# Kernel optimization log

Hardware: AMD Instinct MI355X
Metric: run time of the kernel (lower is better)

The kernel has to match this reference:

```python
import jax, jax.numpy as jnp
import numpy as np

N_NODES = 100000


def _gcn_layer(h, W, b, src, dst, norm, n):
    # h: [N, Fin] -> [N, Fout]; normalized scatter-add aggregation (GCNConv)
    hw = h @ W
    msg = norm[:, None] * hw[src]
    out = jax.ops.segment_sum(msg, dst, num_segments=n)
    return out + b


def setup_inputs() -> dict:
    key = jax.random.key(0)
    k = jax.random.split(key, 10)
    N, E, P, F = N_NODES, 3200000, 500000, 128
    x = jax.random.normal(k[0], (N, F), dtype=jnp.float32)
    edge_index = jax.random.randint(k[1], (2, E), 0, N, dtype=jnp.int64)
    pred_edges = jax.random.randint(k[2], (P, 2), 0, N, dtype=jnp.int64)
    # Glorot-ish init for learned params
    W1 = jax.random.normal(k[3], (F, 16), dtype=jnp.float32) / np.sqrt(F)
    b1 = jnp.zeros((16,), dtype=jnp.float32)
    W2 = jax.random.normal(k[4], (16, 8), dtype=jnp.float32) / np.sqrt(16.0)
    b2 = jnp.zeros((8,), dtype=jnp.float32)
    Wl = jax.random.normal(k[5], (8, 1), dtype=jnp.float32) / np.sqrt(8.0)
    bl = jnp.zeros((1,), dtype=jnp.float32)
    return {"x": x, "edge_index": edge_index, "pred_edges": pred_edges,
            "W1": W1, "b1": b1, "W2": W2, "b2": b2, "Wl": Wl, "bl": bl}


def reference(x, edge_index, pred_edges, W1, b1, W2, b2, Wl, bl):
    n = x.shape[0]
    # GCN norm with self-loops: A_hat = D^{-1/2}(A+I)D^{-1/2}
    loop = jnp.arange(n, dtype=edge_index.dtype)
    src = jnp.concatenate([edge_index[0], loop])
    dst = jnp.concatenate([edge_index[1], loop])
    deg = jax.ops.segment_sum(jnp.ones_like(dst, dtype=x.dtype), dst, num_segments=n)
    dinv = jnp.where(deg > 0, jax.lax.rsqrt(deg), 0.0)
    norm = dinv[src] * dinv[dst]

    h = _gcn_layer(x, W1, b1, src, dst, norm, n)   # [N, 16]
    h = _gcn_layer(h, W2, b2, src, dst, norm, n)   # [N, 8]
    z = jax.nn.sigmoid(h @ Wl + bl)                # [N, 1]
    m = z[pred_edges]                              # [P, 2, 1]
    pred = m[:, 0, 0] * m[:, 1, 0]                 # [P]
    return pred
```

## Files before the change

kernel.cpp:

```cpp
#include <hip/hip_runtime.h>
#include <hip/hip_fp16.h>
#include <math.h>

#define BSHIFT 8
#define BUCK   256
#define TILE   8192
#define CAP    12288

typedef _Float16 f16x2 __attribute__((ext_vector_type(2)));
typedef _Float16 f16x4 __attribute__((ext_vector_type(4)));
typedef _Float16 f16x8 __attribute__((ext_vector_type(8)));
typedef float    f32x4 __attribute__((ext_vector_type(4)));


__global__ __launch_bounds__(256) void k_curinit(int* __restrict__ bcursor, int nbuk) {
    int b = blockIdx.x * 256 + threadIdx.x;
    if (b < nbuk) bcursor[b] = b * CAP;
}

__global__ __launch_bounds__(1024) void k_binscatter(const int* __restrict__ src,
                                                     const int* __restrict__ dst,
                                                     int* __restrict__ bcursor,
                                                     int* __restrict__ binned, int E, int nbuk) {
    __shared__ int            payload[TILE];
    __shared__ unsigned short bid16[TILE];
    __shared__ int cnt[512];
    __shared__ int lstart[512];
    __shared__ int gbase[512];
    __shared__ int wsum[8];
    int t = threadIdx.x;
    int tile0 = blockIdx.x * TILE;
    int tileE = min(TILE, E - tile0);
    if (t < 512) cnt[t] = 0;
    __syncthreads();
    int d[8], s[8];
    int base = t * 8;
    if (base + 8 <= tileE) {
        const int4* d4 = (const int4*)(dst + tile0 + base);
        const int4* s4 = (const int4*)(src + tile0 + base);
        int4 da = d4[0], db = d4[1];
        int4 sa = s4[0], sb = s4[1];
        d[0] = da.x; d[1] = da.y; d[2] = da.z; d[3] = da.w;
        d[4] = db.x; d[5] = db.y; d[6] = db.z; d[7] = db.w;
        s[0] = sa.x; s[1] = sa.y; s[2] = sa.z; s[3] = sa.w;
        s[4] = sb.x; s[5] = sb.y; s[6] = sb.z; s[7] = sb.w;
    } else {
#pragma unroll
        for (int q = 0; q < 8; ++q) {
            int idx = base + q;
            if (idx < tileE) { d[q] = dst[tile0 + idx]; s[q] = src[tile0 + idx]; }
            else d[q] = -1;
        }
    }
#pragma unroll
    for (int q = 0; q < 8; ++q)
        if (d[q] >= 0) atomicAdd(&cnt[d[q] >> BSHIFT], 1);
    __syncthreads();
    int c = 0, ex = 0;
    if (t < 512) {
        c = cnt[t];
        int v = c;
#pragma unroll
        for (int off = 1; off < 64; off <<= 1) {
            int u = __shfl_up(v, off, 64);
            if ((t & 63) >= off) v += u;
        }
        if ((t & 63) == 63) wsum[t >> 6] = v;
        ex = v - c;
    }
    __syncthreads();
    if (t == 0) {
        int run = 0;
#pragma unroll
        for (int w = 0; w < 8; ++w) { int u = wsum[w]; wsum[w] = run; run += u; }
    }
    __syncthreads();
    if (t < 512) {
        ex += wsum[t >> 6];
        gbase[t] = c ? atomicAdd(&bcursor[t], c) : 0;
        lstart[t] = ex;
        cnt[t] = ex;
    }
    __syncthreads();
#pragma unroll
    for (int q = 0; q < 8; ++q) {
        if (d[q] >= 0) {
            int b = d[q] >> BSHIFT;
            int lp = atomicAdd(&cnt[b], 1);
            payload[lp] = ((d[q] & (BUCK - 1)) << 17) | s[q];
            bid16[lp] = (unsigned short)b;
        }
    }
    __syncthreads();
    for (int k = t; k < tileE; k += 1024) {
        int b = bid16[k];
        int ga = gbase[b] + (k - lstart[b]);
        if (ga < (b + 1) * CAP)
            binned[ga] = payload[k];
    }
}

__global__ __launch_bounds__(1024) void k_sortbucket(const int* __restrict__ bcursor,
                                                     const int* __restrict__ binned,
                                                     int* __restrict__ csr_src,
                                                     int* __restrict__ rowstart,
                                                     int* __restrict__ rowend,
                                                     float* __restrict__ dinv, int N) {
    __shared__ int cnt[BUCK];
    __shared__ int cur[BUCK];
    __shared__ int wsum[4];
    int b = blockIdx.x, t = threadIdx.x;
    if (t < BUCK) cnt[t] = 0;
    __syncthreads();
    int beg = b * CAP;
    int end = min(bcursor[b], beg + CAP);
    int v[12];
#pragma unroll
    for (int q = 0; q < 12; ++q) {
        int e = beg + q * 1024 + t;
        v[q] = (e < end) ? binned[e] : -1;
    }
#pragma unroll
    for (int q = 0; q < 12; ++q)
        if (v[q] >= 0) atomicAdd(&cnt[v[q] >> 17], 1);
    __syncthreads();
    int c = 0, ex = 0;
    if (t < BUCK) {
        c = cnt[t];
        int s = c;
#pragma unroll
        for (int off = 1; off < 64; off <<= 1) {
            int u = __shfl_up(s, off, 64);
            if ((t & 63) >= off) s += u;
        }
        if ((t & 63) == 63) wsum[t >> 6] = s;
        ex = s - c;
    }
    __syncthreads();
    if (t == 0) {
        int run = 0;
#pragma unroll
        for (int w = 0; w < 4; ++w) { int u = wsum[w]; wsum[w] = run; run += u; }
    }
    __syncthreads();
    if (t < BUCK) {
        ex += wsum[t >> 6];
        cur[t] = ex;
        int node = b * BUCK + t;
        if (node < N) {
            rowstart[node] = beg + ex;
            rowend[node]   = beg + ex + c;
            dinv[node] = rsqrtf((float)(c + 1));
        }
    }
    __syncthreads();
#pragma unroll
    for (int q = 0; q < 12; ++q) {
        if (v[q] >= 0) {
            int pos = atomicAdd(&cur[v[q] >> 17], 1);
            csr_src[beg + pos] = v[q] & 0x1FFFF;
        }
    }
}


__global__ __launch_bounds__(256) void k_gemm1(const float* __restrict__ x,
                                               const float* __restrict__ W1,
                                               const float* __restrict__ dinv,
                                               __half* __restrict__ hw1h, int N) {
    __shared__ _Float16 sX[64 * 136];
    __shared__ _Float16 sW[16 * 136];
    __shared__ float    sDi[64];
    __shared__ _Float16 sOut[64 * 16];
    int t = threadIdx.x;
    int row0 = blockIdx.x * 64;
    for (int e = t; e < 2048; e += 256) {
        int n = e & 15, k = e >> 4;
        sW[n * 136 + k] = (_Float16)W1[k * 16 + n];
    }
    const float4* x4 = (const float4*)x;
#pragma unroll
    for (int q = 0; q < 8; ++q) {
        int e = q * 256 + t;
        int r = e >> 5, c4 = e & 31;
        int gr = row0 + r;
        float4 v = (gr < N) ? x4[(size_t)gr * 32 + c4] : make_float4(0.f, 0.f, 0.f, 0.f);
        f16x4 hv = {(_Float16)v.x, (_Float16)v.y, (_Float16)v.z, (_Float16)v.w};
        *(f16x4*)&sX[r * 136 + c4 * 4] = hv;
    }
    if (t < 64) sDi[t] = (row0 + t < N) ? dinv[row0 + t] : 0.f;
    __syncthreads();
    int w = t >> 6, l = t & 63;
    int m = l & 15, quad = l >> 4;
    f32x4 acc = {0.f, 0.f, 0.f, 0.f};
#pragma unroll
    for (int kc = 0; kc < 4; ++kc) {
        f16x8 a = *(const f16x8*)&sX[(w * 16 + m) * 136 + kc * 32 + quad * 8];
        f16x8 b = *(const f16x8*)&sW[m * 136 + kc * 32 + quad * 8];
        acc = __builtin_amdgcn_mfma_f32_16x16x32_f16(a, b, acc, 0, 0, 0);
    }
#pragma unroll
    for (int r = 0; r < 4; ++r) {
        int nl = w * 16 + quad * 4 + r;
        sOut[nl * 16 + m] = (_Float16)(acc[r] * sDi[nl]);
    }
    __syncthreads();
    int nn = t >> 2, ch = t & 3;
    int gn = row0 + nn;
    if (gn < N)
        *(float2*)&hw1h[(size_t)gn * 16 + ch * 4] = *(float2*)&sOut[nn * 16 + ch * 4];
}

__global__ __launch_bounds__(256) void k_agg1c(const int* __restrict__ rowstart,
                                               const int* __restrict__ rowend,
                                               const int* __restrict__ csr_src,
                                               const f16x8* __restrict__ hw1v,
                                               const float* __restrict__ W2,
                                               const float* __restrict__ b1,
                                               __half* __restrict__ hw2h, int N) {
    __shared__ float sW[128], sb[16];
    int t = threadIdx.x;
    if (t < 128) sW[t] = W2[t];
    if (t < 16)  sb[t] = b1[t];
    __syncthreads();
    int q = t >> 2, j = t & 3;
    int i = blockIdx.x * 64 + q;
    if (i >= N) return;
    int beg = rowstart[i], end = rowend[i];
    int deg = end - beg;
    float di = rsqrtf((float)(deg + 1));
    float a[16];
#pragma unroll
    for (int d = 0; d < 16; ++d) a[d] = 0.f;
    int nfull = deg >> 4;
    int base0 = beg + 4 * j;
    int s4[4];
    if (nfull > 0) {
#pragma unroll
        for (int m = 0; m < 4; ++m) s4[m] = csr_src[base0 + m];
    }
    for (int ch = 0; ch < nfull; ++ch) {
        f16x8 lo[4], hi[4];
#pragma unroll
        for (int m = 0; m < 4; ++m) {
            lo[m] = hw1v[2 * (size_t)s4[m]];
            hi[m] = hw1v[2 * (size_t)s4[m] + 1];
        }
        int sn[4];
        if (ch + 1 < nfull) {
#pragma unroll
            for (int m = 0; m < 4; ++m) sn[m] = csr_src[base0 + (ch + 1) * 16 + m];
        }
#pragma unroll
        for (int m = 0; m < 4; ++m) {
#pragma unroll
            for (int d = 0; d < 8; ++d) {
                a[d]     += (float)lo[m][d];
                a[8 + d] += (float)hi[m][d];
            }
        }
        if (ch + 1 < nfull) {
#pragma unroll
            for (int m = 0; m < 4; ++m) s4[m] = sn[m];
        }
    }
    if (deg & 15) {
        int cb = beg + nfull * 16 + 4 * j;
        int   sr[4];
        float wr[4];
#pragma unroll
        for (int m = 0; m < 4; ++m) {
            int c = cb + m;
            bool ok = c < end;
            sr[m] = ok ? csr_src[c] : i;
            wr[m] = ok ? 1.f : 0.f;
        }
        f16x8 lo[4], hi[4];
#pragma unroll
        for (int m = 0; m < 4; ++m) {
            lo[m] = hw1v[2 * (size_t)sr[m]];
            hi[m] = hw1v[2 * (size_t)sr[m] + 1];
        }
#pragma unroll
        for (int m = 0; m < 4; ++m) {
#pragma unroll
            for (int d = 0; d < 8; ++d) {
                a[d]     += wr[m] * (float)lo[m][d];
                a[8 + d] += wr[m] * (float)hi[m][d];
            }
        }
    }
    if (j == 0) {
        f16x8 lo = hw1v[2 * (size_t)i];
        f16x8 hi = hw1v[2 * (size_t)i + 1];
#pragma unroll
        for (int d = 0; d < 8; ++d) {
            a[d]     += (float)lo[d];
            a[8 + d] += (float)hi[d];
        }
    }
#pragma unroll
    for (int d = 0; d < 16; ++d) a[d] += __shfl_xor(a[d], 1, 4);
#pragma unroll
    for (int d = 0; d < 16; ++d) a[d] += __shfl_xor(a[d], 2, 4);
    float o0 = 0.f, o1 = 0.f;
#pragma unroll
    for (int k = 0; k < 16; ++k) {
        float hv = di * a[k] + sb[k];
        o0 += hv * sW[k * 8 + 2 * j];
        o1 += hv * sW[k * 8 + 2 * j + 1];
    }
    f16x2 ho = {(_Float16)(di * o0), (_Float16)(di * o1)};
    *(f16x2*)&hw2h[(size_t)i * 8 + 2 * j] = ho;
}

__global__ __launch_bounds__(256) void k_agg2c(const int* __restrict__ rowstart,
                                               const int* __restrict__ rowend,
                                               const int* __restrict__ csr_src,
                                               const f16x8* __restrict__ hw2v,
                                               const float* __restrict__ Wl,
                                               const float* __restrict__ b2,
                                               const float* __restrict__ bl,
                                               float* __restrict__ z, int N) {
    __shared__ float sW[8], sb[8], sbl;
    int t = threadIdx.x;
    if (t < 8) { sW[t] = Wl[t]; sb[t] = b2[t]; }
    if (t == 0) sbl = bl[0];
    __syncthreads();
    int q = t >> 2, j = t & 3;
    int i = blockIdx.x * 64 + q;
    if (i >= N) return;
    int beg = rowstart[i], end = rowend[i];
    int deg = end - beg;
    float di = rsqrtf((float)(deg + 1));
    float a[8];
#pragma unroll
    for (int d = 0; d < 8; ++d) a[d] = 0.f;
    int nfull = deg >> 4;
    int base0 = beg + 4 * j;
    int s4[4];
    if (nfull > 0) {
#pragma unroll
        for (int m = 0; m < 4; ++m) s4[m] = csr_src[base0 + m];
    }
    for (int ch = 0; ch < nfull; ++ch) {
        f16x8 gv[4];
#pragma unroll
        for (int m = 0; m < 4; ++m) gv[m] = hw2v[(size_t)s4[m]];
        int sn[4];
        if (ch + 1 < nfull) {
#pragma unroll
            for (int m = 0; m < 4; ++m) sn[m] = csr_src[base0 + (ch + 1) * 16 + m];
        }
#pragma unroll
        for (int m = 0; m < 4; ++m)
#pragma unroll
            for (int d = 0; d < 8; ++d) a[d] += (float)gv[m][d];
        if (ch + 1 < nfull) {
#pragma unroll
            for (int m = 0; m < 4; ++m) s4[m] = sn[m];
        }
    }
    if (deg & 15) {
        int cb = beg + nfull * 16 + 4 * j;
        int   sr[4];
        float wr[4];
#pragma unroll
        for (int m = 0; m < 4; ++m) {
            int c = cb + m;
            bool ok = c < end;
            sr[m] = ok ? csr_src[c] : i;
            wr[m] = ok ? 1.f : 0.f;
        }
        f16x8 gv[4];
#pragma unroll
        for (int m = 0; m < 4; ++m) gv[m] = hw2v[(size_t)sr[m]];
#pragma unroll
        for (int m = 0; m < 4; ++m)
#pragma unroll
            for (int d = 0; d < 8; ++d) a[d] += wr[m] * (float)gv[m][d];
    }
    if (j == 0) {
        f16x8 self = hw2v[(size_t)i];
#pragma unroll
        for (int d = 0; d < 8; ++d) a[d] += (float)self[d];
    }
#pragma unroll
    for (int d = 0; d < 8; ++d) a[d] += __shfl_xor(a[d], 1, 4);
#pragma unroll
    for (int d = 0; d < 8; ++d) a[d] += __shfl_xor(a[d], 2, 4);
    if (j == 0) {
        float v = 0.f;
#pragma unroll
        for (int d = 0; d < 8; ++d) {
            float h = di * a[d] + sb[d];
            v += h * sW[d];
        }
        z[i] = 1.f / (1.f + __expf(-(v + sbl)));
    }
}

__global__ __launch_bounds__(256) void k_pred(const int2* __restrict__ pe2,
                                              const float* __restrict__ z,
                                              float* __restrict__ out, int P) {
    int p = blockIdx.x * 256 + threadIdx.x;
    if (p < P) {
        int2 e = pe2[p];
        out[p] = z[e.x] * z[e.y];
    }
}


extern "C" void kernel_launch(void* const* d_in, const int* in_sizes, int n_in,
                              void* d_out, int out_size, void* d_ws, size_t ws_size,
                              hipStream_t stream) {
    const float* x  = (const float*)d_in[0];
    const int*   ei = (const int*)d_in[1];
    const int*   pe = (const int*)d_in[2];
    const float* W1 = (const float*)d_in[3];
    const float* b1 = (const float*)d_in[4];
    const float* W2 = (const float*)d_in[5];
    const float* b2 = (const float*)d_in[6];
    const float* Wl = (const float*)d_in[7];
    const float* bl = (const float*)d_in[8];
    float* out = (float*)d_out;

    const int N = in_sizes[0] / 128;
    const int E = in_sizes[1] / 2;
    const int P = in_sizes[2] / 2;
    const int NBUK = (N + BUCK - 1) >> BSHIFT;

    const int* src = ei;
    const int* dst = ei + E;

    float*  ws   = (float*)d_ws;
    float*  dinv = ws;
    __half* hw1h = (__half*)(ws + (size_t)N);
    __half* hw2h = (__half*)(ws + (size_t)9 * N);
    float*  z    = ws + (size_t)13 * N;
    int* rowstart = (int*)(ws + (size_t)14 * N);
    int* rowend   = rowstart + N;
    int* bcursor  = rowend + N;
    int* binned   = bcursor + 512;
    int* csr_src  = binned + (size_t)NBUK * CAP;

    const int B = 256;

    k_curinit<<<(NBUK + B - 1) / B, B, 0, stream>>>(bcursor, NBUK);
    k_binscatter<<<(E + TILE - 1) / TILE, 1024, 0, stream>>>(src, dst, bcursor, binned, E, NBUK);
    k_sortbucket<<<NBUK, 1024, 0, stream>>>(bcursor, binned, csr_src, rowstart, rowend, dinv, N);
    k_gemm1<<<(N + 63) / 64, B, 0, stream>>>(x, W1, dinv, hw1h, N);
    k_agg1c<<<(N + 63) / 64, B, 0, stream>>>(rowstart, rowend, csr_src,
                                             (const f16x8*)hw1h, W2, b1, hw2h, N);
    k_agg2c<<<(N + 63) / 64, B, 0, stream>>>(rowstart, rowend, csr_src,
                                             (const f16x8*)hw2h, Wl, b2, bl, z, N);
    k_pred<<<(P + B - 1) / B, B, 0, stream>>>((const int2*)pe, z, out, P);
}
```

Before: 206.9 us.

## Halve bucket size and tile size for binning and per-bucket sort

Bucket width drops from 256 to 128 nodes, which doubles the bucket count to about 782. The binning tile and block size are halved, and each binscatter thread now handles two bucket counters in the prefix scan. Sortbucket runs with 512 threads on smaller buckets, so more blocks are launched and each uses less shared memory, which should raise occupancy and parallelism. In exchange there are more global bcursor atomics per tile, more scattered partial writes, and a tighter per-bucket capacity margin with CAP at 6144.

```diff
diff --git a/kernel.cpp b/kernel.cpp
--- a/kernel.cpp
+++ b/kernel.cpp
@@ -2,10 +2,10 @@
 #include <hip/hip_fp16.h>
 #include <math.h>
 
-#define BSHIFT 8
-#define BUCK   256
-#define TILE   8192
-#define CAP    12288
+#define BSHIFT 7
+#define BUCK   128
+#define TILE   4096
+#define CAP    6144
 
 typedef _Float16 f16x2 __attribute__((ext_vector_type(2)));
 typedef _Float16 f16x4 __attribute__((ext_vector_type(4)));
@@ -18,20 +18,20 @@
     if (b < nbuk) bcursor[b] = b * CAP;
 }
 
-__global__ __launch_bounds__(1024) void k_binscatter(const int* __restrict__ src,
-                                                     const int* __restrict__ dst,
-                                                     int* __restrict__ bcursor,
-                                                     int* __restrict__ binned, int E, int nbuk) {
+__global__ __launch_bounds__(512) void k_binscatter(const int* __restrict__ src,
+                                                    const int* __restrict__ dst,
+                                                    int* __restrict__ bcursor,
+                                                    int* __restrict__ binned, int E, int nbuk) {
     __shared__ int            payload[TILE];
     __shared__ unsigned short bid16[TILE];
-    __shared__ int cnt[512];
-    __shared__ int lstart[512];
-    __shared__ int gbase[512];
+    __shared__ int cnt[1024];
+    __shared__ int lstart[1024];
+    __shared__ int gbase[1024];
     __shared__ int wsum[8];
     int t = threadIdx.x;
     int tile0 = blockIdx.x * TILE;
     int tileE = min(TILE, E - tile0);
-    if (t < 512) cnt[t] = 0;
+    cnt[t] = 0; cnt[t + 512] = 0;
     __syncthreads();
     int d[8], s[8];
     int base = t * 8;
@@ -56,18 +56,16 @@
     for (int q = 0; q < 8; ++q)
         if (d[q] >= 0) atomicAdd(&cnt[d[q] >> BSHIFT], 1);
     __syncthreads();
-    int c = 0, ex = 0;
-    if (t < 512) {
-        c = cnt[t];
-        int v = c;
-#pragma unroll
-        for (int off = 1; off < 64; off <<= 1) {
-            int u = __shfl_up(v, off, 64);
-            if ((t & 63) >= off) v += u;
-        }
-        if ((t & 63) == 63) wsum[t >> 6] = v;
-        ex = v - c;
-    }
+    int c0 = cnt[2 * t], c1 = cnt[2 * t + 1];
+    int p = c0 + c1;
+    int v = p;
+#pragma unroll
+    for (int off = 1; off < 64; off <<= 1) {
+        int u = __shfl_up(v, off, 64);
+        if ((t & 63) >= off) v += u;
+    }
+    if ((t & 63) == 63) wsum[t >> 6] = v;
+    int ex = v - p;
     __syncthreads();
     if (t == 0) {
         int run = 0;
@@ -75,12 +73,14 @@
         for (int w = 0; w < 8; ++w) { int u = wsum[w]; wsum[w] = run; run += u; }
     }
     __syncthreads();
-    if (t < 512) {
-        ex += wsum[t >> 6];
-        gbase[t] = c ? atomicAdd(&bcursor[t], c) : 0;
-        lstart[t] = ex;
-        cnt[t] = ex;
-    }
+    ex += wsum[t >> 6];
+    lstart[2 * t]     = ex;
+    lstart[2 * t + 1] = ex + c0;
+    gbase[2 * t]     = c0 ? atomicAdd(&bcursor[2 * t], c0) : 0;
+    gbase[2 * t + 1] = c1 ? atomicAdd(&bcursor[2 * t + 1], c1) : 0;
+    __syncthreads();
+    cnt[2 * t]     = ex;
+    cnt[2 * t + 1] = ex + c0;
     __syncthreads();
 #pragma unroll
     for (int q = 0; q < 8; ++q) {
@@ -92,7 +92,7 @@
         }
     }
     __syncthreads();
-    for (int k = t; k < tileE; k += 1024) {
+    for (int k = t; k < tileE; k += 512) {
         int b = bid16[k];
         int ga = gbase[b] + (k - lstart[b]);
         if (ga < (b + 1) * CAP)
@@ -100,15 +100,15 @@
     }
 }
 
-__global__ __launch_bounds__(1024) void k_sortbucket(const int* __restrict__ bcursor,
-                                                     const int* __restrict__ binned,
-                                                     int* __restrict__ csr_src,
-                                                     int* __restrict__ rowstart,
-                                                     int* __restrict__ rowend,
-                                                     float* __restrict__ dinv, int N) {
+__global__ __launch_bounds__(512) void k_sortbucket(const int* __restrict__ bcursor,
+                                                    const int* __restrict__ binned,
+                                                    int* __restrict__ csr_src,
+                                                    int* __restrict__ rowstart,
+                                                    int* __restrict__ rowend,
+                                                    float* __restrict__ dinv, int N) {
     __shared__ int cnt[BUCK];
     __shared__ int cur[BUCK];
-    __shared__ int wsum[4];
+    __shared__ int wsum[2];
     int b = blockIdx.x, t = threadIdx.x;
     if (t < BUCK) cnt[t] = 0;
     __syncthreads();
@@ -117,7 +117,7 @@
     int v[12];
 #pragma unroll
     for (int q = 0; q < 12; ++q) {
-        int e = beg + q * 1024 + t;
+        int e = beg + q * 512 + t;
         v[q] = (e < end) ? binned[e] : -1;
     }
 #pragma unroll
@@ -137,11 +137,7 @@
         ex = s - c;
     }
     __syncthreads();
-    if (t == 0) {
-        int run = 0;
-#pragma unroll
-        for (int w = 0; w < 4; ++w) { int u = wsum[w]; wsum[w] = run; run += u; }
-    }
+    if (t == 0) { int u = wsum[0]; wsum[0] = 0; wsum[1] = u; }
     __syncthreads();
     if (t < BUCK) {
         ex += wsum[t >> 6];
@@ -441,14 +437,14 @@
     int* rowstart = (int*)(ws + (size_t)14 * N);
     int* rowend   = rowstart + N;
     int* bcursor  = rowend + N;
-    int* binned   = bcursor + 512;
+    int* binned   = bcursor + 1024;
     int* csr_src  = binned + (size_t)NBUK * CAP;
 
     const int B = 256;
 
-    k_curinit<<<(NBUK + B - 1) / B, B, 0, stream>>>(bcursor, NBUK);
-    k_binscatter<<<(E + TILE - 1) / TILE, 1024, 0, stream>>>(src, dst, bcursor, binned, E, NBUK);
-    k_sortbucket<<<NBUK, 1024, 0, stream>>>(bcursor, binned, csr_src, rowstart, rowend, dinv, N);
+    k_curinit<<<4, B, 0, stream>>>(bcursor, 1024);
+    k_binscatter<<<(E + TILE - 1) / TILE, 512, 0, stream>>>(src, dst, bcursor, binned, E, NBUK);
+    k_sortbucket<<<NBUK, 512, 0, stream>>>(bcursor, binned, csr_src, rowstart, rowend, dinv, N);
     k_gemm1<<<(N + 63) / 64, B, 0, stream>>>(x, W1, dinv, hw1h, N);
     k_agg1c<<<(N + 63) / 64, B, 0, stream>>>(rowstart, rowend, csr_src,
                                              (const f16x8*)hw1h, W2, b1, hw2h, N);
```

Measured after the change: 230.4 us. 1.11x slower.
